# Kernel tuning notes

Hardware: AMD Instinct MI355X
Metric: run time of the kernel (lower is better)

## Reference

```python
import jax, jax.numpy as jnp
import numpy as np

B, S, D = 2048, 8, 1280
K = 1                 # n_components_remove
HIGH_T = 0.6          # PC1_HIGH_ACTIVITY_THRESHOLD
STORM_T = 0.8         # solar_storm_threshold


def setup_inputs() -> dict:
    key = jax.random.key(0)
    k1, k2 = jax.random.split(key, 2)
    features = jax.random.normal(k1, (B, S, D), dtype=jnp.float32)
    kp_index = jax.random.uniform(k2, (B,), dtype=jnp.float32) * 9.0
    cmr_gate = jnp.ones((1,), dtype=jnp.float32)  # nn.Parameter(torch.ones(1))
    return {"features": features, "kp_index": kp_index, "cmr_gate": cmr_gate}


def reference(features, kp_index, cmr_gate):
    # Per-sample standardization over the feature axis (numpy std, ddof=0)
    mu = features.mean(axis=2, keepdims=True)            # (B, S, 1)
    sigma = features.std(axis=2, keepdims=True) + 1e-8   # (B, S, 1)
    fn = (features - mu) / sigma                         # (B, S, D)

    # Batched thin SVD of the (S, D) normalized feature matrix
    U, sv, Vt = jnp.linalg.svd(fn, full_matrices=False)  # (B,S,S), (B,S), (B,S,D)
    var = sv * sv
    pc1_ratio = var[:, 0] / (var.sum(axis=-1) + 1e-8)    # (B,)

    # solar_flag: 0 normal, 1 high activity, 2 storm
    solar_flag = (pc1_ratio >= HIGH_T).astype(jnp.int32) + (pc1_ratio >= STORM_T).astype(jnp.int32)

    # Rank-K reconstruction of the common-mode (solar) component
    low = jnp.einsum('bsk,bk,bkd->bsd', U[:, :, :K], sv[:, :K], Vt[:, :K, :])
    clean = (fn - low) * sigma + mu                      # de-normalized cleaned features

    # Kp-gating: amplify CMR when Kp >= 5
    kp_gate = 1.0 + 0.5 * (kp_index >= 5.0).astype(features.dtype)[:, None, None]
    clean = features + kp_gate * (clean - features)

    # Learnable gate
    gate = jax.nn.sigmoid(cmr_gate)[0]
    features_clean = features + gate * (clean - features)
    return features_clean, pc1_ratio, solar_flag
```

## Files before the change

### kernel.cpp

```cpp
#include <hip/hip_runtime.h>
#include <math.h>

#define SV 8
#define DV 1280
#define THREADS 256
#define F4PERBATCH ((SV*DV)/4)
#define PER_T (F4PERBATCH/THREADS)

__global__ __launch_bounds__(THREADS)
void cmr_kernel(const float* __restrict__ feat,
                const float* __restrict__ kp,
                const float* __restrict__ cmr_gate,
                float* __restrict__ out,
                int Bn)
{
    __shared__ __align__(16) float tile[SV * DV];
    __shared__ __align__(16) float pbuf[DV];
    __shared__ float gsc[4][36];
    __shared__ float csum[36];
    __shared__ float muS[SV], sigS[SV], rsigS[SV];
    __shared__ float coefS[SV], aS[SV];
    __shared__ float bconstS;
    __shared__ float pc1S, flagS;

    const int b = blockIdx.x;
    const int tid = threadIdx.x;

    const float4* __restrict__ src4 = (const float4*)(feat + (size_t)b * SV * DV);
    float4* tile4 = (float4*)tile;
#pragma unroll
    for (int k = 0; k < PER_T; ++k)
        tile4[tid + THREADS * k] = src4[tid + THREADS * k];
    __syncthreads();

    {
        const int r = tid >> 5;
        const int l = tid & 31;
        float s = 0.f, ss = 0.f;
#pragma unroll
        for (int k = 0; k < DV / 32; ++k) {
            float v = tile[r * DV + l + 32 * k];
            s += v; ss = fmaf(v, v, ss);
        }
#pragma unroll
        for (int m = 16; m >= 1; m >>= 1) {
            s  += __shfl_xor(s,  m);
            ss += __shfl_xor(ss, m);
        }
        if (l == 0) {
            float mu  = s / (float)DV;
            float var = fmaxf(ss / (float)DV - mu * mu, 0.f);
            float sig = sqrtf(var) + 1e-8f;
            muS[r] = mu; sigS[r] = sig; rsigS[r] = 1.f / sig;
        }
    }
    __syncthreads();

    float acc[36];
#pragma unroll
    for (int k = 0; k < 36; ++k) acc[k] = 0.f;
    for (int k = 0; k < DV / THREADS; ++k) {
        const int d = tid + THREADS * k;
        float f[8];
#pragma unroll
        for (int s = 0; s < 8; ++s) f[s] = tile[s * DV + d];
        int idx = 0;
#pragma unroll
        for (int i = 0; i < 8; ++i)
#pragma unroll
            for (int j = i; j < 8; ++j) { acc[idx] = fmaf(f[i], f[j], acc[idx]); ++idx; }
    }
#pragma unroll
    for (int m = 32; m >= 1; m >>= 1)
#pragma unroll
        for (int k = 0; k < 36; ++k) acc[k] += __shfl_xor(acc[k], m);
    {
        const int wave = tid >> 6;
        if ((tid & 63) == 0)
#pragma unroll
            for (int k = 0; k < 36; ++k) gsc[wave][k] = acc[k];
    }
    __syncthreads();
    if (tid < 36)
        csum[tid] = gsc[0][tid] + gsc[1][tid] + gsc[2][tid] + gsc[3][tid];
    __syncthreads();

    if (tid < 64) {
        const int i = tid >> 3, j = tid & 7;
        const int a_ = (i < j) ? i : j;
        const int b_ = (i < j) ? j : i;
        const int t_ = 8 * a_ - (a_ * (a_ - 1)) / 2 + (b_ - a_);
        const float G = (csum[t_] - (float)DV * muS[i] * muS[j]) * rsigS[i] * rsigS[j];

        float tr = (i == j) ? G : 0.f;
#pragma unroll
        for (int m = 32; m >= 1; m >>= 1) tr += __shfl_xor(tr, m);

        float A = G;
        float mx = fabsf(A);
#pragma unroll
        for (int m = 32; m >= 1; m >>= 1) mx = fmaxf(mx, __shfl_xor(mx, m));
        A = A / fmaxf(mx, 1e-37f);
        for (int t = 0; t < 16; ++t) {
            float nb = 0.f;
#pragma unroll
            for (int k = 0; k < 8; ++k)
                nb = fmaf(__shfl(A, i * 8 + k), __shfl(A, k * 8 + j), nb);
            float m2 = fabsf(nb);
#pragma unroll
            for (int m = 32; m >= 1; m >>= 1) m2 = fmaxf(m2, __shfl_xor(m2, m));
            A = nb / fmaxf(m2, 1e-37f);
        }

        float cn = A * A;
#pragma unroll
        for (int m = 8; m <= 32; m <<= 1) cn += __shfl_xor(cn, m);
        float best = cn; int bj = j;
#pragma unroll
        for (int m = 1; m <= 4; m <<= 1) {
            float ov = __shfl_xor(best, m);
            int   oj = __shfl_xor(bj, m);
            if (ov > best || (ov == best && oj < bj)) { best = ov; bj = oj; }
        }
        float u = __shfl(A, i * 8 + bj);
        float nn = u * u;
#pragma unroll
        for (int m = 8; m <= 32; m <<= 1) nn += __shfl_xor(nn, m);
        u *= rsqrtf(fmaxf(nn, 1e-37f));

        for (int it = 0; it < 2; ++it) {
            float yp = G * __shfl(u, j * 8);
#pragma unroll
            for (int m = 1; m <= 4; m <<= 1) yp += __shfl_xor(yp, m);
            float ny = yp * yp;
#pragma unroll
            for (int m = 8; m <= 32; m <<= 1) ny += __shfl_xor(ny, m);
            u = yp * rsqrtf(fmaxf(ny, 1e-37f));
        }

        float lp = G * u * __shfl(u, j * 8);
#pragma unroll
        for (int m = 32; m >= 1; m >>= 1) lp += __shfl_xor(lp, m);
        const float lam = lp;

        const float gate    = 1.f / (1.f + expf(-cmr_gate[0]));
        const float kp_gate = (kp[b] >= 5.0f) ? 1.5f : 1.0f;
        const float Gt      = gate * kp_gate;

        if (j == 0) {
            coefS[i] = Gt * sigS[i] * u;
            aS[i]    = u * rsigS[i];
        }
        float bp = (j == 0) ? u * rsigS[i] * muS[i] : 0.f;
#pragma unroll
        for (int m = 32; m >= 1; m >>= 1) bp += __shfl_xor(bp, m);
        if (tid == 0) {
            bconstS = bp;
            const float pc1 = lam / (tr + 1e-8f);
            pc1S  = pc1;
            flagS = (pc1 >= 0.6f ? 1.f : 0.f) + (pc1 >= 0.8f ? 1.f : 0.f);
        }
    }
    __syncthreads();

    for (int k = 0; k < DV / THREADS; ++k) {
        const int d = tid + THREADS * k;
        float p = -bconstS;
#pragma unroll
        for (int s = 0; s < 8; ++s) p = fmaf(aS[s], tile[s * DV + d], p);
        pbuf[d] = p;
    }
    __syncthreads();

    float4* __restrict__ dst4 = (float4*)(out + (size_t)b * SV * DV);
    const float4* pbuf4 = (const float4*)pbuf;
#pragma unroll
    for (int k = 0; k < PER_T; ++k) {
        const int e4 = tid + THREADS * k;
        const int s  = e4 / (DV / 4);
        const int dg = e4 % (DV / 4);
        const float c = coefS[s];
        float4 f = tile4[e4];
        float4 p = pbuf4[dg];
        float4 o;
        o.x = fmaf(-c, p.x, f.x);
        o.y = fmaf(-c, p.y, f.y);
        o.z = fmaf(-c, p.z, f.z);
        o.w = fmaf(-c, p.w, f.w);
        dst4[e4] = o;
    }

    if (tid == 0) {
        out[(size_t)Bn * SV * DV + b]      = pc1S;
        out[(size_t)Bn * SV * DV + Bn + b] = flagS;
    }
}

extern "C" void kernel_launch(void* const* d_in, const int* in_sizes, int n_in,
                              void* d_out, int out_size, void* d_ws, size_t ws_size,
                              hipStream_t stream) {
    const float* feat = (const float*)d_in[0];
    const float* kp   = (const float*)d_in[1];
    const float* gate = (const float*)d_in[2];
    const int Bn = in_sizes[0] / (SV * DV);
    cmr_kernel<<<Bn, THREADS, 0, stream>>>(feat, kp, gate, (float*)d_out, Bn);
}
```

Before: 199.2 us.

## Split into wave-per-sample stats and apply kernels, dropping LDS tile

Replaces the single block-per-sample kernel that staged the whole sample in shared memory with two kernels, each using one 64-lane wave per sample. The first computes row sums and the Gram matrix straight from global memory, runs trace-normalized power iteration in registers, and writes per-sample coefficients to a workspace. The second rereads the features and applies the rank-1 correction with float4 accesses. This removes the 40KB LDS footprint and block-level syncs so more waves fit per CU, but the input is read from global memory twice and an extra launch is added.

```diff
diff --git a/kernel.cpp b/kernel.cpp
--- a/kernel.cpp
+++ b/kernel.cpp
@@ -1,198 +1,190 @@
 #include <hip/hip_runtime.h>
 #include <math.h>
 
+
 #define SV 8
 #define DV 1280
-#define THREADS 256
-#define F4PERBATCH ((SV*DV)/4)
-#define PER_T (F4PERBATCH/THREADS)
-
-__global__ __launch_bounds__(THREADS)
-void cmr_kernel(const float* __restrict__ feat,
-                const float* __restrict__ kp,
-                const float* __restrict__ cmr_gate,
-                float* __restrict__ out,
-                int Bn)
+#define BSTRIDE (SV*DV)
+#define WSS 17
+
+__global__ __launch_bounds__(256)
+void cmr_stats_kernel(const float* __restrict__ feat,
+                      const float* __restrict__ kp,
+                      const float* __restrict__ cmr_gate,
+                      float* __restrict__ cws,
+                      float* __restrict__ out,
+                      int Bn)
 {
-    __shared__ __align__(16) float tile[SV * DV];
-    __shared__ __align__(16) float pbuf[DV];
-    __shared__ float gsc[4][36];
-    __shared__ float csum[36];
-    __shared__ float muS[SV], sigS[SV], rsigS[SV];
-    __shared__ float coefS[SV], aS[SV];
-    __shared__ float bconstS;
-    __shared__ float pc1S, flagS;
-
-    const int b = blockIdx.x;
-    const int tid = threadIdx.x;
-
-    const float4* __restrict__ src4 = (const float4*)(feat + (size_t)b * SV * DV);
-    float4* tile4 = (float4*)tile;
-#pragma unroll
-    for (int k = 0; k < PER_T; ++k)
-        tile4[tid + THREADS * k] = src4[tid + THREADS * k];
-    __syncthreads();
-
+    const int lane = threadIdx.x & 63;
+    const int b = blockIdx.x * 4 + (threadIdx.x >> 6);
+
+    const float* __restrict__ fb = feat + (size_t)b * BSTRIDE;
+
+    float Sr[8], C[36];
+#pragma unroll
+    for (int s = 0; s < 8; ++s) Sr[s] = 0.f;
+#pragma unroll
+    for (int t = 0; t < 36; ++t) C[t] = 0.f;
+
+#pragma unroll
+    for (int k = 0; k < DV / 64; ++k) {
+        const int d = lane + 64 * k;
+        float f[8];
+#pragma unroll
+        for (int s = 0; s < 8; ++s) f[s] = fb[s * DV + d];
+#pragma unroll
+        for (int s = 0; s < 8; ++s) Sr[s] += f[s];
+        int idx = 0;
+#pragma unroll
+        for (int i = 0; i < 8; ++i)
+#pragma unroll
+            for (int j = i; j < 8; ++j) { C[idx] = fmaf(f[i], f[j], C[idx]); ++idx; }
+    }
+#pragma unroll
+    for (int m = 32; m >= 1; m >>= 1) {
+#pragma unroll
+        for (int s = 0; s < 8; ++s) Sr[s] += __shfl_xor(Sr[s], m);
+#pragma unroll
+        for (int t = 0; t < 36; ++t) C[t] += __shfl_xor(C[t], m);
+    }
+
+    const int i = lane >> 3, j = lane & 7;
+    const int a_ = (i < j) ? i : j;
+    const int b_ = (i < j) ? j : i;
+    const int tii = 8 * i - (i * (i - 1)) / 2;
+    const int tjj = 8 * j - (j * (j - 1)) / 2;
+    const int tij = 8 * a_ - (a_ * (a_ - 1)) / 2 + (b_ - a_);
+
+    float Ci = 0.f, Cj = 0.f, Cij = 0.f, Si = 0.f, Sj = 0.f;
+#pragma unroll
+    for (int t = 0; t < 36; ++t) {
+        Ci  = (t == tii) ? C[t] : Ci;
+        Cj  = (t == tjj) ? C[t] : Cj;
+        Cij = (t == tij) ? C[t] : Cij;
+    }
+#pragma unroll
+    for (int s = 0; s < 8; ++s) {
+        Si = (s == i) ? Sr[s] : Si;
+        Sj = (s == j) ? Sr[s] : Sj;
+    }
+    const float invD = 1.f / (float)DV;
+    const float mui = Si * invD, muj = Sj * invD;
+    const float vari = fmaxf(Ci * invD - mui * mui, 0.f);
+    const float varj = fmaxf(Cj * invD - muj * muj, 0.f);
+    const float sigi = sqrtf(vari) + 1e-8f;
+    const float sigj = sqrtf(varj) + 1e-8f;
+    const float rsigi = 1.f / sigi, rsigj = 1.f / sigj;
+    const float G = ((Cij - (float)DV * mui * muj) * rsigi) * rsigj;
+
+    float tr = (i == j) ? G : 0.f;
+#pragma unroll
+    for (int m = 32; m >= 1; m >>= 1) tr += __shfl_xor(tr, m);
+    const float trs = fmaxf(tr, 1e-30f);
+
+    float A = G / trs;
+#pragma unroll
+    for (int t = 0; t < 14; ++t) {
+        float nb = 0.f;
+#pragma unroll
+        for (int k = 0; k < 8; ++k)
+            nb = fmaf(__shfl(A, i * 8 + k), __shfl(A, k * 8 + j), nb);
+        float dg = (i == j) ? nb : 0.f;
+#pragma unroll
+        for (int m = 32; m >= 1; m >>= 1) dg += __shfl_xor(dg, m);
+        A = nb / fmaxf(dg, 1e-30f);
+    }
+
+    float dv = (i == j) ? A : -1.f;
+    int bj = j;
+#pragma unroll
+    for (int m = 32; m >= 1; m >>= 1) {
+        float ov = __shfl_xor(dv, m);
+        int   oj = __shfl_xor(bj, m);
+        if (ov > dv) { dv = ov; bj = oj; }
+    }
+    float u = __shfl(A, i * 8 + bj);
     {
-        const int r = tid >> 5;
-        const int l = tid & 31;
-        float s = 0.f, ss = 0.f;
-#pragma unroll
-        for (int k = 0; k < DV / 32; ++k) {
-            float v = tile[r * DV + l + 32 * k];
-            s += v; ss = fmaf(v, v, ss);
+        float nn = (j == 0) ? u * u : 0.f;
+#pragma unroll
+        for (int m = 32; m >= 1; m >>= 1) nn += __shfl_xor(nn, m);
+        u *= rsqrtf(fmaxf(nn, 1e-30f));
+    }
+#pragma unroll
+    for (int it = 0; it < 2; ++it) {
+        float y = G * __shfl(u, j * 8);
+#pragma unroll
+        for (int m = 1; m <= 4; m <<= 1) y += __shfl_xor(y, m);
+        float ny = (j == 0) ? y * y : 0.f;
+#pragma unroll
+        for (int m = 32; m >= 1; m >>= 1) ny += __shfl_xor(ny, m);
+        u = y * rsqrtf(fmaxf(ny, 1e-30f));
+    }
+    float lp = G * u * __shfl(u, j * 8);
+#pragma unroll
+    for (int m = 32; m >= 1; m >>= 1) lp += __shfl_xor(lp, m);
+    const float pc1 = lp / (tr + 1e-8f);
+
+    const float gate = 1.f / (1.f + expf(-cmr_gate[0]));
+    const float kpg  = (kp[b] >= 5.0f) ? 1.5f : 1.0f;
+    const float Gt   = gate * kpg;
+
+    float bcp = (j == 0) ? u * rsigi * mui : 0.f;
+#pragma unroll
+    for (int m = 32; m >= 1; m >>= 1) bcp += __shfl_xor(bcp, m);
+
+    float* wsb = cws + (size_t)b * WSS;
+    if (j == 0) {
+        wsb[i]     = u * rsigi;
+        wsb[8 + i] = Gt * sigi * u;
+    }
+    if (lane == 0) {
+        wsb[16] = bcp;
+        out[(size_t)Bn * BSTRIDE + b] = pc1;
+        const float flag = (pc1 >= 0.6f ? 1.f : 0.f) + (pc1 >= 0.8f ? 1.f : 0.f);
+        out[(size_t)Bn * BSTRIDE + Bn + b] = flag;
+    }
+}
+
+__global__ __launch_bounds__(256)
+void cmr_apply_kernel(const float* __restrict__ feat,
+                      const float* __restrict__ cws,
+                      float* __restrict__ out)
+{
+    const int lane = threadIdx.x & 63;
+    const int b = blockIdx.x * 4 + (threadIdx.x >> 6);
+
+    const float* __restrict__ wsb = cws + (size_t)b * WSS;
+    float a[8], c[8];
+#pragma unroll
+    for (int s = 0; s < 8; ++s) { a[s] = wsb[s]; c[s] = wsb[8 + s]; }
+    const float bc = wsb[16];
+
+    const float4* __restrict__ f4 = (const float4*)(feat + (size_t)b * BSTRIDE);
+    float4* __restrict__ o4 = (float4*)(out + (size_t)b * BSTRIDE);
+
+#pragma unroll
+    for (int k = 0; k < 5; ++k) {
+        const int d4 = lane + 64 * k;
+        float4 f[8];
+#pragma unroll
+        for (int s = 0; s < 8; ++s) f[s] = f4[s * (DV / 4) + d4];
+        float4 p = make_float4(-bc, -bc, -bc, -bc);
+#pragma unroll
+        for (int s = 0; s < 8; ++s) {
+            p.x = fmaf(a[s], f[s].x, p.x);
+            p.y = fmaf(a[s], f[s].y, p.y);
+            p.z = fmaf(a[s], f[s].z, p.z);
+            p.w = fmaf(a[s], f[s].w, p.w);
         }
 #pragma unroll
-        for (int m = 16; m >= 1; m >>= 1) {
-            s  += __shfl_xor(s,  m);
-            ss += __shfl_xor(ss, m);
+        for (int s = 0; s < 8; ++s) {
+            float4 o;
+            o.x = fmaf(-c[s], p.x, f[s].x);
+            o.y = fmaf(-c[s], p.y, f[s].y);
+            o.z = fmaf(-c[s], p.z, f[s].z);
+            o.w = fmaf(-c[s], p.w, f[s].w);
+            o4[s * (DV / 4) + d4] = o;
         }
-        if (l == 0) {
-            float mu  = s / (float)DV;
-            float var = fmaxf(ss / (float)DV - mu * mu, 0.f);
-            float sig = sqrtf(var) + 1e-8f;
-            muS[r] = mu; sigS[r] = sig; rsigS[r] = 1.f / sig;
-        }
-    }
-    __syncthreads();
-
-    float acc[36];
-#pragma unroll
-    for (int k = 0; k < 36; ++k) acc[k] = 0.f;
-    for (int k = 0; k < DV / THREADS; ++k) {
-        const int d = tid + THREADS * k;
-        float f[8];
-#pragma unroll
-        for (int s = 0; s < 8; ++s) f[s] = tile[s * DV + d];
-        int idx = 0;
-#pragma unroll
-        for (int i = 0; i < 8; ++i)
-#pragma unroll
-            for (int j = i; j < 8; ++j) { acc[idx] = fmaf(f[i], f[j], acc[idx]); ++idx; }
-    }
-#pragma unroll
-    for (int m = 32; m >= 1; m >>= 1)
-#pragma unroll
-        for (int k = 0; k < 36; ++k) acc[k] += __shfl_xor(acc[k], m);
-    {
-        const int wave = tid >> 6;
-        if ((tid & 63) == 0)
-#pragma unroll
-            for (int k = 0; k < 36; ++k) gsc[wave][k] = acc[k];
-    }
-    __syncthreads();
-    if (tid < 36)
-        csum[tid] = gsc[0][tid] + gsc[1][tid] + gsc[2][tid] + gsc[3][tid];
-    __syncthreads();
-
-    if (tid < 64) {
-        const int i = tid >> 3, j = tid & 7;
-        const int a_ = (i < j) ? i : j;
-        const int b_ = (i < j) ? j : i;
-        const int t_ = 8 * a_ - (a_ * (a_ - 1)) / 2 + (b_ - a_);
-        const float G = (csum[t_] - (float)DV * muS[i] * muS[j]) * rsigS[i] * rsigS[j];
-
-        float tr = (i == j) ? G : 0.f;
-#pragma unroll
-        for (int m = 32; m >= 1; m >>= 1) tr += __shfl_xor(tr, m);
-
-        float A = G;
-        float mx = fabsf(A);
-#pragma unroll
-        for (int m = 32; m >= 1; m >>= 1) mx = fmaxf(mx, __shfl_xor(mx, m));
-        A = A / fmaxf(mx, 1e-37f);
-        for (int t = 0; t < 16; ++t) {
-            float nb = 0.f;
-#pragma unroll
-            for (int k = 0; k < 8; ++k)
-                nb = fmaf(__shfl(A, i * 8 + k), __shfl(A, k * 8 + j), nb);
-            float m2 = fabsf(nb);
-#pragma unroll
-            for (int m = 32; m >= 1; m >>= 1) m2 = fmaxf(m2, __shfl_xor(m2, m));
-            A = nb / fmaxf(m2, 1e-37f);
-        }
-
-        float cn = A * A;
-#pragma unroll
-        for (int m = 8; m <= 32; m <<= 1) cn += __shfl_xor(cn, m);
-        float best = cn; int bj = j;
-#pragma unroll
-        for (int m = 1; m <= 4; m <<= 1) {
-            float ov = __shfl_xor(best, m);
-            int   oj = __shfl_xor(bj, m);
-            if (ov > best || (ov == best && oj < bj)) { best = ov; bj = oj; }
-        }
-        float u = __shfl(A, i * 8 + bj);
-        float nn = u * u;
-#pragma unroll
-        for (int m = 8; m <= 32; m <<= 1) nn += __shfl_xor(nn, m);
-        u *= rsqrtf(fmaxf(nn, 1e-37f));
-
-        for (int it = 0; it < 2; ++it) {
-            float yp = G * __shfl(u, j * 8);
-#pragma unroll
-            for (int m = 1; m <= 4; m <<= 1) yp += __shfl_xor(yp, m);
-            float ny = yp * yp;
-#pragma unroll
-            for (int m = 8; m <= 32; m <<= 1) ny += __shfl_xor(ny, m);
-            u = yp * rsqrtf(fmaxf(ny, 1e-37f));
-        }
-
-        float lp = G * u * __shfl(u, j * 8);
-#pragma unroll
-        for (int m = 32; m >= 1; m >>= 1) lp += __shfl_xor(lp, m);
-        const float lam = lp;
-
-        const float gate    = 1.f / (1.f + expf(-cmr_gate[0]));
-        const float kp_gate = (kp[b] >= 5.0f) ? 1.5f : 1.0f;
-        const float Gt      = gate * kp_gate;
-
-        if (j == 0) {
-            coefS[i] = Gt * sigS[i] * u;
-            aS[i]    = u * rsigS[i];
-        }
-        float bp = (j == 0) ? u * rsigS[i] * muS[i] : 0.f;
-#pragma unroll
-        for (int m = 32; m >= 1; m >>= 1) bp += __shfl_xor(bp, m);
-        if (tid == 0) {
-            bconstS = bp;
-            const float pc1 = lam / (tr + 1e-8f);
-            pc1S  = pc1;
-            flagS = (pc1 >= 0.6f ? 1.f : 0.f) + (pc1 >= 0.8f ? 1.f : 0.f);
-        }
-    }
-    __syncthreads();
-
-    for (int k = 0; k < DV / THREADS; ++k) {
-        const int d = tid + THREADS * k;
-        float p = -bconstS;
-#pragma unroll
-        for (int s = 0; s < 8; ++s) p = fmaf(aS[s], tile[s * DV + d], p);
-        pbuf[d] = p;
-    }
-    __syncthreads();
-
-    float4* __restrict__ dst4 = (float4*)(out + (size_t)b * SV * DV);
-    const float4* pbuf4 = (const float4*)pbuf;
-#pragma unroll
-    for (int k = 0; k < PER_T; ++k) {
-        const int e4 = tid + THREADS * k;
-        const int s  = e4 / (DV / 4);
-        const int dg = e4 % (DV / 4);
-        const float c = coefS[s];
-        float4 f = tile4[e4];
-        float4 p = pbuf4[dg];
-        float4 o;
-        o.x = fmaf(-c, p.x, f.x);
-        o.y = fmaf(-c, p.y, f.y);
-        o.z = fmaf(-c, p.z, f.z);
-        o.w = fmaf(-c, p.w, f.w);
-        dst4[e4] = o;
-    }
-
-    if (tid == 0) {
-        out[(size_t)Bn * SV * DV + b]      = pc1S;
-        out[(size_t)Bn * SV * DV + Bn + b] = flagS;
     }
 }
 
@@ -202,6 +194,10 @@
     const float* feat = (const float*)d_in[0];
     const float* kp   = (const float*)d_in[1];
     const float* gate = (const float*)d_in[2];
-    const int Bn = in_sizes[0] / (SV * DV);
-    cmr_kernel<<<Bn, THREADS, 0, stream>>>(feat, kp, gate, (float*)d_out, Bn);
+    float* out = (float*)d_out;
+    float* cws = (float*)d_ws;
+    const int Bn = in_sizes[0] / BSTRIDE;
+
+    cmr_stats_kernel<<<Bn / 4, 256, 0, stream>>>(feat, kp, gate, cws, out, Bn);
+    cmr_apply_kernel<<<Bn / 4, 256, 0, stream>>>(feat, cws, out);
 }
```

Result: faster. 179.8 us (-9.7%).
